# Optimization experiments

Hardware: AMD Instinct MI355X
Metric: run time of the kernel (lower is better)

## Reference

```python
import jax, jax.numpy as jnp
import numpy as np

B, L = 2, 4096
EMBED_DIM, NUM_HEADS, WINDOW = 1024, 16, 256
NUM_EXPERTS, TOP_K, FF_HIDDEN = 8, 2, 4096
ENTROPY_W, MAX_USAGE = 0.1, 0.3


def setup_inputs() -> dict:
    key = jax.random.key(0)
    ks = jax.random.split(key, 10)
    s = 0.02
    C, F, E = EMBED_DIM, FF_HIDDEN, NUM_EXPERTS
    return {
        "x": jax.random.normal(ks[0], (B, L, C), jnp.float32),
        "g1": jnp.ones((C,), jnp.float32), "b1": jnp.zeros((C,), jnp.float32),
        "g2": jnp.ones((C,), jnp.float32), "b2": jnp.zeros((C,), jnp.float32),
        "g3": jnp.ones((C,), jnp.float32), "b3": jnp.zeros((C,), jnp.float32),
        "Wqkv": jax.random.normal(ks[1], (C, 3 * C), jnp.float32) * s, "bqkv": jnp.zeros((3 * C,), jnp.float32),
        "Wo": jax.random.normal(ks[2], (C, C), jnp.float32) * s, "bo": jnp.zeros((C,), jnp.float32),
        "conv_w": jax.random.normal(ks[3], (C, C, 3), jnp.float32) * s, "conv_b": jnp.zeros((C,), jnp.float32),
        "gate_W": jax.random.normal(ks[4], (C, E), jnp.float32) * s, "gate_b": jnp.zeros((E,), jnp.float32),
        "expert_W": jax.random.normal(ks[5], (E, C, C), jnp.float32) * s, "expert_b": jnp.zeros((E, C), jnp.float32),
        "ff_W1": jax.random.normal(ks[6], (C, F), jnp.float32) * s, "ff_b1": jnp.zeros((F,), jnp.float32),
        "ff_W2": jax.random.normal(ks[7], (F, C), jnp.float32) * s, "ff_b2": jnp.zeros((C,), jnp.float32),
    }


def _ln(x, g, b):
    mu = x.mean(-1, keepdims=True)
    var = ((x - mu) ** 2).mean(-1, keepdims=True)
    return (x - mu) * jax.lax.rsqrt(var + 1e-5) * g + b


def _local_attn(x, Wqkv, bqkv, Wo, bo):
    # Faithful port of the unfold-based overlapping-window attention
    Bsz, Ln, C = x.shape
    hd = C // NUM_HEADS
    pad = (-Ln) % WINDOW
    xp = jnp.pad(x, ((0, 0), (0, pad), (0, 0)))
    Lp = Ln + pad
    qkv = (xp @ Wqkv + bqkv).reshape(Bsz, Lp, 3, NUM_HEADS, hd).transpose(2, 0, 3, 1, 4)
    q, k, v = qkv[0], qkv[1], qkv[2]  # [B,H,Lp,hd]
    step = WINDOW // 2  # bidirectional=True -> overlapping windows
    nw = (Lp - WINDOW) // step + 1
    idx = (jnp.arange(nw) * step)[:, None] + jnp.arange(WINDOW)[None, :]  # [nw,w]

    def win(t):
        # torch unfold(dim=2,size=w,step) puts window on LAST axis -> [B,H,nw,hd,w]
        return jnp.swapaxes(t[:, :, idx, :], -1, -2)

    qw, kw, vw = win(q), win(k), win(v)
    # q @ k^T over the window axis (exactly what the torch code computes)
    attn = jax.nn.softmax(jnp.einsum('bhnds,bhnes->bhnde', qw, kw) * hd ** -0.5, axis=-1)
    o = jnp.einsum('bhnde,bhnes->bhnds', attn, vw)  # [B,H,nw,hd,w]
    o = o.reshape(Bsz, NUM_HEADS, nw * WINDOW, hd).transpose(0, 2, 1, 3).reshape(Bsz, nw * WINDOW, C)
    return (o @ Wo + bo)[:, :Ln]


def _dconv(x, w, b):
    # Conv1d(C,C,k=3,dilation=2,padding='same'); w is [O,I,K]
    y = jax.lax.conv_general_dilated(jnp.swapaxes(x, 1, 2), w, (1,), 'SAME',
                                     rhs_dilation=(2,), dimension_numbers=('NCH', 'OIH', 'NCH'))
    return jnp.swapaxes(y + b[None, :, None], 1, 2)


def _moe(x, gW, gb, eW, eb):
    Bsz, S, C = x.shape
    N = Bsz * S
    xf = x.reshape(N, C)
    probs = jax.nn.softmax(xf @ gW + gb, axis=-1)
    entropy = -jnp.sum(probs * jnp.log(probs + 1e-10), axis=-1).mean()
    topk_p, topk_i = jax.lax.top_k(probs, TOP_K)  # [N,K]
    # dense-equivalent top-k dispatch: out[n] = sum_k p_k * expert_{i_k}(x_n)
    eo = jnp.einsum('nc,ech->neh', xf, eW) + eb  # [N,E,C]
    combine = jnp.zeros((N, NUM_EXPERTS), xf.dtype).at[jnp.arange(N)[:, None], topk_i].add(topk_p)
    out = jnp.einsum('neh,ne->nh', eo, combine)
    counts = jnp.zeros((NUM_EXPERTS,), jnp.float32).at[topk_i.reshape(-1)].add(1.0)
    penalty = jnp.sum(jax.nn.relu(counts / N - MAX_USAGE))
    return out.reshape(Bsz, S, C), ENTROPY_W * entropy + penalty


def reference(x, g1, b1, g2, b2, g3, b3, Wqkv, bqkv, Wo, bo, conv_w, conv_b,
              gate_W, gate_b, expert_W, expert_b, ff_W1, ff_b1, ff_W2, ff_b2):
    x = x + _local_attn(_ln(x, g1, b1), Wqkv, bqkv, Wo, bo)
    x = x + _dconv(_ln(x, g2, b2), conv_w, conv_b)
    moe_out, aux = _moe(_ln(x, g3, b3), gate_W, gate_b, expert_W, expert_b)
    x = x + moe_out
    x = x + (jax.nn.gelu(x @ ff_W1 + ff_b1, approximate=False) @ ff_W2 + ff_b2)
    return x, aux
```

## Files before the change

### kernel.cpp

```cpp
#include <hip/hip_runtime.h>
#include <cmath>

typedef _Float16 f16;
typedef __attribute__((ext_vector_type(8))) _Float16 f16x8;
typedef __attribute__((ext_vector_type(4))) _Float16 f16x4;
typedef __attribute__((ext_vector_type(4))) float f32x4;

struct TileInfo { int m0, mcnt, e, pad; };

__device__ __forceinline__ void gload16(const void* g, void* l) {
  __builtin_amdgcn_global_load_lds((const __attribute__((address_space(1))) void*)g,
                                   (__attribute__((address_space(3))) void*)l, 16, 0, 0);
}

__device__ __forceinline__ float fast_gelu(float u) {
  const float c = u * (0.7978845608028654f + 0.0356774081f * u * u);
  const float t = fminf(2.0f * c, 80.0f);
  const float e = __expf(t);
  return u * (e * __builtin_amdgcn_rcpf(e + 1.0f));
}

template<int NPASS, int MODE, int EPI>
__global__ __launch_bounds__(256)
void gemm_kernel(const f16* __restrict__ Ah, const f16* __restrict__ Al, int lda,
                 const f16* __restrict__ Bh, const f16* __restrict__ Bl, int ldb,
                 const float* __restrict__ bias, const float* __restrict__ res,
                 float* __restrict__ outf, f16* __restrict__ outh, int ldo, int K,
                 const int* __restrict__ rowmap, const TileInfo* __restrict__ table,
                 const char* __restrict__ zbuf) {
  __shared__ __align__(16) char lds[65536];

  const int tid  = threadIdx.x;
  const int wave = tid >> 6;
  const int lane = tid & 63;

  int m0, mcnt, eidx = 0;
  if (MODE == 2) {
    TileInfo ti = table[blockIdx.x];
    if (ti.mcnt <= 0) return;
    m0 = ti.m0; mcnt = ti.mcnt; eidx = ti.e;
  } else { m0 = blockIdx.x * 128; mcnt = 128; }
  const int n0 = blockIdx.y * 128;

  const f16* Bh_ = Bh;
  const float* bias_ = bias;
  size_t adelta = 0, bdelta = 0;
  if (NPASS == 3) {
    adelta = (size_t)((const char*)Al - (const char*)Ah);
    bdelta = (size_t)((const char*)Bl - (const char*)Bh);
  }
  if (MODE == 2) { Bh_ += ((size_t)eidx << 20); bias_ += eidx * 1024; }

  f32x4 acc[4][4] = {};
  const int wm  = (wave >> 1) * 64;
  const int wn  = (wave & 1) * 64;
  const int fr  = lane & 15;
  const int kgb = (lane >> 4) * 16;
  const int wuni = wave * 1024;

  const int sr    = tid / 8;
  const int cbyte = (tid % 8) * 16;

  if constexpr (NPASS == 1) {
    const char* aSrc[4];
    const char* bSrc[4];
    #pragma unroll
    for (int r = 0; r < 4; ++r) {
      const int mr  = sr + r * 32;
      const int cbs = cbyte ^ ((mr & 7) << 4);
      int gi = m0 + ((mr < mcnt) ? mr : (mcnt - 1));
      if (MODE == 1 || MODE == 2) gi = rowmap[gi];
      aSrc[r] = (const char*)Ah + (size_t)gi * lda * 2 + cbs;
      bSrc[r] = (const char*)Bh_ + (size_t)(n0 + mr) * ldb * 2 + cbs;
    }
    const int NT = K / 64;
    #pragma unroll
    for (int r = 0; r < 4; ++r) {
      gload16(aSrc[r], lds + r * 4096 + wuni);
      gload16(bSrc[r], lds + 16384 + r * 4096 + wuni);
    }
    #pragma unroll
    for (int r = 0; r < 4; ++r) {
      gload16(aSrc[r] + 128, lds + 32768 + r * 4096 + wuni);
      gload16(bSrc[r] + 128, lds + 32768 + 16384 + r * 4096 + wuni);
    }
    asm volatile("s_waitcnt vmcnt(8)" ::: "memory");
    __builtin_amdgcn_s_barrier();

    for (int kt = 0; kt < NT; ++kt) {
      const int c = kt & 1;
      const char* LAp = lds + c * 32768;
      const char* LBp = LAp + 16384;
      f16x8 ah[2][4], bh[2][4];
      #pragma unroll
      for (int kk = 0; kk < 2; ++kk) {
        #pragma unroll
        for (int i = 0; i < 4; ++i) {
          const int ar = wm + i * 16 + fr;
          ah[kk][i] = *(const f16x8*)(LAp + ar * 128 + ((kk * 64 + kgb) ^ ((ar & 7) << 4)));
          const int br = wn + i * 16 + fr;
          bh[kk][i] = *(const f16x8*)(LBp + br * 128 + ((kk * 64 + kgb) ^ ((br & 7) << 4)));
        }
      }
      asm volatile("s_waitcnt lgkmcnt(0)" ::: "memory");
      __builtin_amdgcn_s_barrier();
      if (kt + 2 < NT) {
        const size_t ko = (size_t)(kt + 2) * 128;
        #pragma unroll
        for (int r = 0; r < 4; ++r) {
          gload16(aSrc[r] + ko, lds + c * 32768 + r * 4096 + wuni);
          gload16(bSrc[r] + ko, lds + c * 32768 + 16384 + r * 4096 + wuni);
        }
      }
      #pragma unroll
      for (int kk = 0; kk < 2; ++kk)
        #pragma unroll
        for (int i = 0; i < 4; ++i)
          #pragma unroll
          for (int j = 0; j < 4; ++j)
            acc[i][j] = __builtin_amdgcn_mfma_f32_16x16x32_f16(ah[kk][i], bh[kk][j], acc[i][j], 0, 0, 0);
      if (kt + 2 < NT) asm volatile("s_waitcnt vmcnt(8)" ::: "memory");
      else             asm volatile("s_waitcnt vmcnt(0)" ::: "memory");
      __builtin_amdgcn_s_barrier();
    }
  } else {
    const char* aSrcB[4]; const char* bSrcB[4];
    int aRowC[4], aCbs[4];
    #pragma unroll
    for (int r = 0; r < 4; ++r) {
      const int mr  = sr + r * 32;
      const int cbs = cbyte ^ ((mr & 7) << 4);
      int gi = m0 + mr;
      if (MODE == 1) gi = rowmap[gi];
      if (MODE == 3) { aRowC[r] = gi; aCbs[r] = cbs; aSrcB[r] = nullptr; }
      else           { aSrcB[r] = (const char*)Ah + (size_t)gi * lda * 2 + cbs; aRowC[r] = 0; aCbs[r] = 0; }
      bSrcB[r] = (const char*)Bh_ + (size_t)(n0 + mr) * ldb * 2 + cbs;
    }
    for (int k0 = 0; k0 < K; k0 += 64) {
      #pragma unroll
      for (int r = 0; r < 4; ++r) {
        const char* as; const char* asl;
        if (MODE == 3) {
          const int tap = k0 >> 10;
          const int kc  = k0 & 1023;
          const int tok = aRowC[r] & 4095;
          const int stk = tok + (tap - 1) * 2;
          if (stk >= 0 && stk < 4096) {
            as  = (const char*)Ah + (size_t)(aRowC[r] + (tap - 1) * 2) * 2048 + kc * 2 + aCbs[r];
            asl = as + adelta;
          } else { as = zbuf; asl = zbuf; }
        } else {
          as  = aSrcB[r] + (size_t)k0 * 2;
          asl = as + adelta;
        }
        gload16(as,  lds + 0     + r * 4096 + wuni);
        gload16(asl, lds + 16384 + r * 4096 + wuni);
        const char* bs = bSrcB[r] + (size_t)k0 * 2;
        gload16(bs,          lds + 32768 + r * 4096 + wuni);
        gload16(bs + bdelta, lds + 49152 + r * 4096 + wuni);
      }
      __syncthreads();
      #pragma unroll
      for (int kk = 0; kk < 2; ++kk) {
        f16x8 ah[4], al[4], bh[4], bl[4];
        #pragma unroll
        for (int i = 0; i < 4; ++i) {
          const int ar = wm + i * 16 + fr;
          const int ao = ar * 128 + ((kk * 64 + kgb) ^ ((ar & 7) << 4));
          ah[i] = *(const f16x8*)(lds + ao);
          al[i] = *(const f16x8*)(lds + 16384 + ao);
          const int br = wn + i * 16 + fr;
          const int bo = br * 128 + ((kk * 64 + kgb) ^ ((br & 7) << 4));
          bh[i] = *(const f16x8*)(lds + 32768 + bo);
          bl[i] = *(const f16x8*)(lds + 49152 + bo);
        }
        #pragma unroll
        for (int i = 0; i < 4; ++i) {
          #pragma unroll
          for (int j = 0; j < 4; ++j) {
            acc[i][j] = __builtin_amdgcn_mfma_f32_16x16x32_f16(ah[i], bh[j], acc[i][j], 0, 0, 0);
            acc[i][j] = __builtin_amdgcn_mfma_f32_16x16x32_f16(ah[i], bl[j], acc[i][j], 0, 0, 0);
            acc[i][j] = __builtin_amdgcn_mfma_f32_16x16x32_f16(al[i], bh[j], acc[i][j], 0, 0, 0);
          }
        }
      }
      __syncthreads();
    }
  }

  #pragma unroll
  for (int i = 0; i < 4; ++i) {
    const int mb = wm + i * 16 + (lane >> 4) * 4;
    #pragma unroll
    for (int j = 0; j < 4; ++j) {
      const int nc = n0 + wn + j * 16 + fr;
      const float bv = bias_[nc];
      #pragma unroll
      for (int q = 0; q < 4; ++q) {
        const int ml = mb + q;
        if (MODE == 2 && ml >= mcnt) continue;
        const size_t orow = (size_t)(m0 + ml);
        float v = acc[i][j][q] + bv;
        if (EPI == 1) v += res[orow * ldo + nc];
        if (EPI == 3) v = fast_gelu(v);
        if (EPI <= 1) outf[orow * ldo + nc] = v;
        else          outh[orow * ldo + nc] = (f16)v;
      }
    }
  }
}

template<int WLO, int WGATE, int COMPACT>
__global__ __launch_bounds__(256)
void ln_kernel(const float* __restrict__ x, const float* __restrict__ g, const float* __restrict__ b,
               f16* __restrict__ oh, f16* __restrict__ ol,
               const float* __restrict__ gW, const float* __restrict__ gb,
               float* __restrict__ logits) {
  const int row = blockIdx.x;
  const int srow = COMPACT ? ((row < 2176) ? row : row + 1920) : row;
  const int t = threadIdx.x;
  const float4 v = ((const float4*)(x + (size_t)srow * 1024))[t];
  float s  = v.x + v.y + v.z + v.w;
  float ss = v.x * v.x + v.y * v.y + v.z * v.z + v.w * v.w;
  #pragma unroll
  for (int off = 32; off; off >>= 1) { s += __shfl_down(s, off, 64); ss += __shfl_down(ss, off, 64); }
  __shared__ float red[8];
  if ((t & 63) == 0) { red[t >> 6] = s; red[(t >> 6) + 4] = ss; }
  __syncthreads();
  s  = red[0] + red[1] + red[2] + red[3];
  ss = red[4] + red[5] + red[6] + red[7];
  const float mu  = s * (1.0f / 1024.0f);
  const float var = ss * (1.0f / 1024.0f) - mu * mu;
  const float inv = 1.0f / sqrtf(var + 1e-5f);
  const float4 gv = ((const float4*)g)[t];
  const float4 bv = ((const float4*)b)[t];
  float y[4];
  y[0] = (v.x - mu) * inv * gv.x + bv.x;
  y[1] = (v.y - mu) * inv * gv.y + bv.y;
  y[2] = (v.z - mu) * inv * gv.z + bv.z;
  y[3] = (v.w - mu) * inv * gv.w + bv.w;
  f16x4 hv;
  #pragma unroll
  for (int u = 0; u < 4; ++u) hv[u] = (f16)y[u];
  *(f16x4*)(oh + (size_t)row * 1024 + t * 4) = hv;
  if (WLO) {
    f16x4 lv;
    #pragma unroll
    for (int u = 0; u < 4; ++u) lv[u] = (f16)(y[u] - (float)hv[u]);
    *(f16x4*)(ol + (size_t)row * 1024 + t * 4) = lv;
  }
  if (WGATE) {
    const float* gr = gW + (size_t)(t * 4) * 8;
    float lg[8];
    #pragma unroll
    for (int e = 0; e < 8; ++e)
      lg[e] = y[0] * gr[e] + y[1] * gr[8 + e] + y[2] * gr[16 + e] + y[3] * gr[24 + e];
    #pragma unroll
    for (int m = 1; m < 64; m <<= 1)
      #pragma unroll
      for (int e = 0; e < 8; ++e) lg[e] += __shfl_xor(lg[e], m, 64);
    __shared__ float gred[4][8];
    if ((t & 63) == 0) {
      #pragma unroll
      for (int e = 0; e < 8; ++e) gred[t >> 6][e] = lg[e];
    }
    __syncthreads();
    if (t < 8)
      logits[(size_t)row * 8 + t] = gred[0][t] + gred[1][t] + gred[2][t] + gred[3][t] + gb[t];
  }
}

__global__ __launch_bounds__(512, 4)
void attn_kernel(const float* __restrict__ qkv, f16* __restrict__ oh, f16* __restrict__ ol) {
  __shared__ __align__(16) char sm[81920];
  const int bid = blockIdx.x;
  const int b = bid >> 8, h = (bid >> 4) & 15, n = bid & 15;
  const int t = threadIdx.x;
  const size_t rowbase = (size_t)(b * 2176 + n * 128);
  const char* qg = (const char*)(qkv + rowbase * 3072 + h * 64);
  const char* kg = qg + 4096;
  const char* vg = qg + 8192;

  const int srow = t >> 4;
  const int scol = (t & 15) * 16;
  const int wuni = (t >> 6) * 1024;

  const int dt = t >> 4;
  const int et = t & 15;
  float pacc[2][4] = {};

  for (int r = 0; r < 2; ++r) {
    #pragma unroll
    for (int p = 0; p < 4; ++p) {
      const size_t off = (size_t)(r * 128 + p * 32 + srow) * 12288 + scol;
      gload16(qg + off, sm + p * 8192 + wuni);
      gload16(kg + off, sm + 32768 + p * 8192 + wuni);
    }
    __syncthreads();
    #pragma unroll 4
    for (int s = 0; s < 128; ++s) {
      const float2 q2 = *(const float2*)(sm + s * 256 + dt * 8);
      const f32x4 k4 = *(const f32x4*)(sm + 32768 + s * 256 + et * 16);
      #pragma unroll
      for (int z = 0; z < 4; ++z) {
        pacc[0][z] += q2.x * k4[z];
        pacc[1][z] += q2.y * k4[z];
      }
    }
    __syncthreads();
  }

  #pragma unroll
  for (int i = 0; i < 2; ++i) {
    #pragma unroll
    for (int z = 0; z < 4; ++z) pacc[i][z] *= 0.125f;
    float m = fmaxf(fmaxf(pacc[i][0], pacc[i][1]), fmaxf(pacc[i][2], pacc[i][3]));
    m = fmaxf(m, __shfl_xor(m, 1, 16));
    m = fmaxf(m, __shfl_xor(m, 2, 16));
    m = fmaxf(m, __shfl_xor(m, 4, 16));
    m = fmaxf(m, __shfl_xor(m, 8, 16));
    float den = 0.0f;
    #pragma unroll
    for (int z = 0; z < 4; ++z) { pacc[i][z] = __expf(pacc[i][z] - m); den += pacc[i][z]; }
    den += __shfl_xor(den, 1, 16);
    den += __shfl_xor(den, 2, 16);
    den += __shfl_xor(den, 4, 16);
    den += __shfl_xor(den, 8, 16);
    const float dinv = 1.0f / den;
    f32x4 pv;
    #pragma unroll
    for (int z = 0; z < 4; ++z) pv[z] = pacc[i][z] * dinv;
    *(f32x4*)(sm + 65536 + (dt * 2 + i) * 256 + et * 16) = pv;
  }

  const int dt2 = t & 15;
  const int st  = t >> 4;
  const int ch  = h * 64 + (st & 15) * 4;
  const size_t rb2 = (size_t)(b * 4096 + n * 256);

  for (int c = 0; c < 2; ++c) {
    __syncthreads();
    #pragma unroll
    for (int p = 0; p < 4; ++p) {
      const size_t off = (size_t)(c * 128 + p * 32 + srow) * 12288 + scol;
      gload16(vg + off, sm + p * 8192 + wuni);
    }
    __syncthreads();
    float o[16];
    #pragma unroll
    for (int u = 0; u < 16; ++u) o[u] = 0.0f;
    #pragma unroll 2
    for (int e4 = 0; e4 < 16; ++e4) {
      f32x4 p4[4], v4[4];
      #pragma unroll
      for (int i = 0; i < 4; ++i)
        p4[i] = *(const f32x4*)(sm + 65536 + (dt2 * 4 + i) * 256 + e4 * 16);
      #pragma unroll
      for (int j = 0; j < 4; ++j)
        v4[j] = *(const f32x4*)(sm + (st * 4 + j) * 256 + e4 * 16);
      #pragma unroll
      for (int j = 0; j < 4; ++j)
        #pragma unroll
        for (int i = 0; i < 4; ++i) {
          o[j * 4 + i] += v4[j][0] * p4[i][0] + v4[j][1] * p4[i][1]
                        + v4[j][2] * p4[i][2] + v4[j][3] * p4[i][3];
        }
    }
    const int rq = c * 2 + (st >> 4);
    #pragma unroll
    for (int i = 0; i < 4; ++i) {
      const size_t row = rb2 + (size_t)(dt2 * 4 + i) * 4 + rq;
      f16x4 hv, lv;
      #pragma unroll
      for (int j = 0; j < 4; ++j) {
        const float val = o[j * 4 + i];
        hv[j] = (f16)val;
        lv[j] = (f16)(val - (float)hv[j]);
      }
      *(f16x4*)(oh + row * 1024 + ch) = hv;
      *(f16x4*)(ol + row * 1024 + ch) = lv;
    }
  }
}

template<int SPLIT>
__global__ __launch_bounds__(256)
void transpose_kernel(const float* __restrict__ in, int R, int Cc,
                      f16* __restrict__ oh, f16* __restrict__ ol) {
  __shared__ float tile[32][33];
  const size_t mat = (size_t)blockIdx.z * R * Cc;
  in += mat; oh += mat; if (SPLIT) ol += mat;
  const int tx = threadIdx.x & 31, ty = threadIdx.x >> 5;
  const int c = blockIdx.x * 32 + tx;
  #pragma unroll
  for (int j = 0; j < 32; j += 8) {
    const int r = blockIdx.y * 32 + ty + j;
    tile[ty + j][tx] = in[(size_t)r * Cc + c];
  }
  __syncthreads();
  const int rT = blockIdx.y * 32 + tx;
  #pragma unroll
  for (int j = 0; j < 32; j += 8) {
    const int cT = blockIdx.x * 32 + ty + j;
    const float v = tile[tx][ty + j];
    const f16 hv = (f16)v;
    oh[(size_t)cT * R + rT] = hv;
    if (SPLIT) ol[(size_t)cT * R + rT] = (f16)(v - (float)hv);
  }
}

__global__ __launch_bounds__(256)
void convw_kernel(const float* __restrict__ w, f16* __restrict__ oh, f16* __restrict__ ol) {
  const int id = blockIdx.x * 256 + threadIdx.x;
  const int o = id >> 10, i = id & 1023;
  const float* ws = w + (size_t)o * 3072 + i * 3;
  #pragma unroll
  for (int tap = 0; tap < 3; ++tap) {
    const float v = ws[tap];
    const f16 hv = (f16)v;
    const size_t oi = (size_t)o * 3072 + tap * 1024 + i;
    oh[oi] = hv;
    ol[oi] = (f16)(v - (float)hv);
  }
}

__global__ __launch_bounds__(256)
void gatefin_kernel(const float* __restrict__ logits, float* __restrict__ top2p,
                    int* __restrict__ top2i, float* __restrict__ ent,
                    int* __restrict__ counts) {
  __shared__ int hist[8];
  const int t = threadIdx.x;
  if (t < 8) hist[t] = 0;
  __syncthreads();
  const int token = blockIdx.x * 256 + t;
  float lg[8];
  const float4 l0 = ((const float4*)(logits + (size_t)token * 8))[0];
  const float4 l1 = ((const float4*)(logits + (size_t)token * 8))[1];
  lg[0] = l0.x; lg[1] = l0.y; lg[2] = l0.z; lg[3] = l0.w;
  lg[4] = l1.x; lg[5] = l1.y; lg[6] = l1.z; lg[7] = l1.w;
  int i0 = 0; float v0 = lg[0];
  #pragma unroll
  for (int e = 1; e < 8; ++e) if (lg[e] > v0) { v0 = lg[e]; i0 = e; }
  int i1 = 0; float v1 = -1e30f;
  #pragma unroll
  for (int e = 0; e < 8; ++e) if (e != i0 && lg[e] > v1) { v1 = lg[e]; i1 = e; }
  float den = 0.0f; float pr[8];
  #pragma unroll
  for (int e = 0; e < 8; ++e) { pr[e] = __expf(lg[e] - v0); den += pr[e]; }
  const float dinv = 1.0f / den;
  float H = 0.0f, p0 = 0.0f, p1 = 0.0f;
  #pragma unroll
  for (int e = 0; e < 8; ++e) {
    const float p = pr[e] * dinv;
    H -= p * __logf(p + 1e-10f);
    if (e == i0) p0 = p;
    if (e == i1) p1 = p;
  }
  ent[token] = H;
  top2p[token * 2] = p0; top2p[token * 2 + 1] = p1;
  top2i[token * 2] = i0; top2i[token * 2 + 1] = i1;
  atomicAdd(&hist[i0], 1);
  atomicAdd(&hist[i1], 1);
  __syncthreads();
  if (t < 8) atomicAdd(&counts[t], hist[t]);
}

__global__ __launch_bounds__(256)
void scan_kernel(const float* __restrict__ ent, const int* __restrict__ counts,
                 int* __restrict__ offs, TileInfo* __restrict__ table, float* __restrict__ auxout) {
  __shared__ float red[256];
  const int t = threadIdx.x;
  float s = 0.0f;
  for (int k = 0; k < 32; ++k) s += ent[t + (k << 8)];
  red[t] = s; __syncthreads();
  for (int hh = 128; hh > 0; hh >>= 1) { if (t < hh) red[t] += red[t + hh]; __syncthreads(); }
  if (t == 0) {
    const float entmean = red[0] * (1.0f / 8192.0f);
    float pen = 0.0f; int off = 0; int nt = 0;
    for (int e = 0; e < 8; ++e) {
      const int c = counts[e];
      offs[e] = off;
      for (int m = 0; m < c; m += 128) {
        table[nt].m0 = off + m;
        table[nt].mcnt = (c - m < 128) ? (c - m) : 128;
        table[nt].e = e; table[nt].pad = 0;
        ++nt;
      }
      off += c;
      const float fr = (float)c * (1.0f / 8192.0f) - 0.3f;
      pen += (fr > 0.0f) ? fr : 0.0f;
    }
    for (; nt < 160; ++nt) { table[nt].m0 = 0; table[nt].mcnt = 0; table[nt].e = 0; table[nt].pad = 0; }
    auxout[0] = 0.1f * entmean + pen;
  }
}

__global__ __launch_bounds__(256)
void scatter_kernel(const int* __restrict__ top2i, const int* __restrict__ offs,
                    int* __restrict__ fill, int* __restrict__ moe_rows,
                    int* __restrict__ row2slot) {
  __shared__ int hist[8];
  __shared__ int base[8];
  const int t = threadIdx.x;
  if (t < 8) hist[t] = 0;
  __syncthreads();
  const int id = blockIdx.x * 256 + t;
  const int e = top2i[id];
  const int myrank = atomicAdd(&hist[e], 1);
  __syncthreads();
  if (t < 8) base[t] = atomicAdd(&fill[t], hist[t]);
  __syncthreads();
  const int row = offs[e] + base[e] + myrank;
  moe_rows[row] = id >> 1;
  row2slot[id] = row;
}

__global__ __launch_bounds__(256)
void combine_kernel(const float* __restrict__ x2, const f16* __restrict__ eo,
                    const float* __restrict__ top2p, const int* __restrict__ row2slot,
                    float* __restrict__ x3, f16* __restrict__ x3h) {
  const int n = blockIdx.x;
  const int t = threadIdx.x;
  const int r0 = row2slot[n * 2], r1 = row2slot[n * 2 + 1];
  const float p0 = top2p[n * 2], p1 = top2p[n * 2 + 1];
  const float4 xv = ((const float4*)(x2 + (size_t)n * 1024))[t];
  const f16x4 e0 = ((const f16x4*)(eo + (size_t)r0 * 1024))[t];
  const f16x4 e1 = ((const f16x4*)(eo + (size_t)r1 * 1024))[t];
  float4 o;
  o.x = xv.x + p0 * (float)e0[0] + p1 * (float)e1[0];
  o.y = xv.y + p0 * (float)e0[1] + p1 * (float)e1[1];
  o.z = xv.z + p0 * (float)e0[2] + p1 * (float)e1[2];
  o.w = xv.w + p0 * (float)e0[3] + p1 * (float)e1[3];
  ((float4*)(x3 + (size_t)n * 1024))[t] = o;
  f16x4 hv; hv[0] = (f16)o.x; hv[1] = (f16)o.y; hv[2] = (f16)o.z; hv[3] = (f16)o.w;
  ((f16x4*)(x3h + (size_t)n * 1024))[t] = hv;
}

extern "C" void kernel_launch(void* const* d_in, const int* in_sizes, int n_in,
                              void* d_out, int out_size, void* d_ws, size_t ws_size,
                              hipStream_t stream) {
  (void)in_sizes; (void)n_in; (void)out_size; (void)ws_size;
  const float* x     = (const float*)d_in[0];
  const float* g1    = (const float*)d_in[1];
  const float* b1    = (const float*)d_in[2];
  const float* g2    = (const float*)d_in[3];
  const float* b2    = (const float*)d_in[4];
  const float* g3    = (const float*)d_in[5];
  const float* b3    = (const float*)d_in[6];
  const float* Wqkv  = (const float*)d_in[7];
  const float* bqkv  = (const float*)d_in[8];
  const float* Wo    = (const float*)d_in[9];
  const float* bo    = (const float*)d_in[10];
  const float* convw = (const float*)d_in[11];
  const float* convb = (const float*)d_in[12];
  const float* gateW = (const float*)d_in[13];
  const float* gateb = (const float*)d_in[14];
  const float* expW  = (const float*)d_in[15];
  const float* expb  = (const float*)d_in[16];
  const float* ffW1  = (const float*)d_in[17];
  const float* ffb1  = (const float*)d_in[18];
  const float* ffW2  = (const float*)d_in[19];
  const float* ffb2  = (const float*)d_in[20];
  float* out = (float*)d_out;

  char* W = (char*)d_ws;
  f16* wqkvT_h = (f16*)(W + 0);
  f16* wqkvT_l = (f16*)(W + 6291456);
  f16* woT_h   = (f16*)(W + 12582912);
  f16* woT_l   = (f16*)(W + 14680064);
  f16* wcvT_h  = (f16*)(W + 16777216);
  f16* wcvT_l  = (f16*)(W + 23068672);
  f16* wexpT   = (f16*)(W + 29360128);
  f16* wff1T   = (f16*)(W + 46137344);
  f16* wff2T   = (f16*)(W + 54525952);
  char* META   = W + 62914560;
  int* counts    = (int*)(META);
  int* fill      = (int*)(META + 32);
  int* offs      = (int*)(META + 64);
  TileInfo* table = (TileInfo*)(META + 128);
  char* zbuf     = META + 3072;
  float* ent     = (float*)(META + 24576);
  float* top2p   = (float*)(META + 57344);
  int* top2i     = (int*)(META + 122880);
  int* moe_rows  = (int*)(META + 188416);
  int* row2slot  = (int*)(META + 253952);
  float* logits  = (float*)(META + 327680);
  char* SA = W + 63963136;
  char* SB = W + 97517568;
  char* SC = W + 164626432;
  char* SD = W + 198180864;
  char* SE = W + 231735296;

  f16* ln1h = (f16*)SA;            f16* ln1l = (f16*)(SA + 16777216);
  f16* ln2h = ln1h;                f16* ln2l = ln1l;
  f16* ln3h = ln1h;                f16* x3h  = (f16*)(SA + 16777216);
  float* qkvbuf = (float*)SB;
  float* x2buf  = (float*)SB;
  f16*   hbuf   = (f16*)SB;
  f16* attnh = (f16*)SC;           f16* attnl = (f16*)(SC + 16777216);
  float* x1 = (float*)SD;
  f16* eobuf = (f16*)SD;
  float* x3 = (float*)SE;

  hipMemsetAsync((void*)META, 0, 4096, stream);

  dim3 blk(256);
  transpose_kernel<1><<<dim3(96, 32, 1), blk, 0, stream>>>(Wqkv, 1024, 3072, wqkvT_h, wqkvT_l);
  transpose_kernel<1><<<dim3(32, 32, 1), blk, 0, stream>>>(Wo, 1024, 1024, woT_h, woT_l);
  convw_kernel<<<4096, blk, 0, stream>>>(convw, wcvT_h, wcvT_l);
  transpose_kernel<0><<<dim3(32, 32, 8), blk, 0, stream>>>(expW, 1024, 1024, wexpT, nullptr);
  transpose_kernel<0><<<dim3(128, 32, 1), blk, 0, stream>>>(ffW1, 1024, 4096, wff1T, nullptr);
  transpose_kernel<0><<<dim3(32, 128, 1), blk, 0, stream>>>(ffW2, 4096, 1024, wff2T, nullptr);

  ln_kernel<1, 0, 1><<<4352, blk, 0, stream>>>(x, g1, b1, ln1h, ln1l, nullptr, nullptr, nullptr);
  gemm_kernel<3, 0, 0><<<dim3(34, 24), blk, 0, stream>>>(ln1h, ln1l, 1024, wqkvT_h, wqkvT_l, 1024,
      bqkv, nullptr, qkvbuf, nullptr, 3072, 1024, nullptr, nullptr, nullptr);
  attn_kernel<<<512, dim3(512), 0, stream>>>(qkvbuf, attnh, attnl);
  gemm_kernel<3, 0, 1><<<dim3(64, 8), blk, 0, stream>>>(attnh, attnl, 1024, woT_h, woT_l, 1024,
      bo, x, x1, nullptr, 1024, 1024, nullptr, nullptr, nullptr);
  ln_kernel<1, 0, 0><<<8192, blk, 0, stream>>>(x1, g2, b2, ln2h, ln2l, nullptr, nullptr, nullptr);
  gemm_kernel<3, 3, 1><<<dim3(64, 8), blk, 0, stream>>>(ln2h, ln2l, 1024, wcvT_h, wcvT_l, 3072,
      convb, x1, x2buf, nullptr, 1024, 3072, nullptr, nullptr, zbuf);
  ln_kernel<0, 1, 0><<<8192, blk, 0, stream>>>(x2buf, g3, b3, ln3h, nullptr, gateW, gateb, logits);
  gatefin_kernel<<<32, blk, 0, stream>>>(logits, top2p, top2i, ent, counts);
  scan_kernel<<<1, blk, 0, stream>>>(ent, counts, offs, table, out + 8388608);
  scatter_kernel<<<64, blk, 0, stream>>>(top2i, offs, fill, moe_rows, row2slot);
  gemm_kernel<1, 2, 2><<<dim3(136, 8), blk, 0, stream>>>(ln3h, nullptr, 1024, wexpT, nullptr, 1024,
      expb, nullptr, nullptr, eobuf, 1024, 1024, moe_rows, table, nullptr);
  combine_kernel<<<8192, blk, 0, stream>>>(x2buf, eobuf, top2p, row2slot, x3, x3h);
  gemm_kernel<1, 0, 3><<<dim3(64, 32), blk, 0, stream>>>(x3h, nullptr, 1024, wff1T, nullptr, 1024,
      ffb1, nullptr, nullptr, hbuf, 4096, 1024, nullptr, nullptr, nullptr);
  gemm_kernel<1, 0, 1><<<dim3(64, 8), blk, 0, stream>>>(hbuf, nullptr, 4096, wff2T, nullptr, 4096,
      ffb2, x3, out, nullptr, 1024, 4096, nullptr, nullptr, nullptr);
}
```

Measured before the change: 743.9 us.

## Fuse weight prep, LN1 and meta zeroing into one kernel; drop fp32 x3

Merges the six weight transpose/convert launches, the first layernorm and the metadata memset into a single prep kernel that dispatches on block index. It also merges the scan and scatter kernels into one launch. Separately, the combine step no longer writes an fp32 x3; the final FF2 GEMM reads the fp16 x3h as its residual through a new epilogue mode. This cuts launch overhead and an 32MB fp32 write/read, at the cost of residual precision (fp16 residual added to the output).

```diff
diff --git a/kernel.cpp b/kernel.cpp
--- a/kernel.cpp
+++ b/kernel.cpp
@@ -202,29 +202,29 @@
         const size_t orow = (size_t)(m0 + ml);
         float v = acc[i][j][q] + bv;
         if (EPI == 1) v += res[orow * ldo + nc];
+        if (EPI == 4) v += (float)((const f16*)res)[orow * ldo + nc];
         if (EPI == 3) v = fast_gelu(v);
-        if (EPI <= 1) outf[orow * ldo + nc] = v;
-        else          outh[orow * ldo + nc] = (f16)v;
-      }
-    }
-  }
-}
-
-template<int WLO, int WGATE, int COMPACT>
-__global__ __launch_bounds__(256)
-void ln_kernel(const float* __restrict__ x, const float* __restrict__ g, const float* __restrict__ b,
-               f16* __restrict__ oh, f16* __restrict__ ol,
-               const float* __restrict__ gW, const float* __restrict__ gb,
-               float* __restrict__ logits) {
-  const int row = blockIdx.x;
-  const int srow = COMPACT ? ((row < 2176) ? row : row + 1920) : row;
+        if (EPI <= 1 || EPI == 4) outf[orow * ldo + nc] = v;
+        else                      outh[orow * ldo + nc] = (f16)v;
+      }
+    }
+  }
+}
+
+template<int WLO, int WGATE>
+__device__ __forceinline__ void ln_body(const float* __restrict__ x, int srow, int row,
+    const float* __restrict__ g, const float* __restrict__ b,
+    f16* __restrict__ oh, f16* __restrict__ ol,
+    const float* __restrict__ gW, const float* __restrict__ gb,
+    float* __restrict__ logits, char* smraw) {
+  float* red  = (float*)smraw;
+  float* gred = (float*)(smraw + 32);
   const int t = threadIdx.x;
   const float4 v = ((const float4*)(x + (size_t)srow * 1024))[t];
   float s  = v.x + v.y + v.z + v.w;
   float ss = v.x * v.x + v.y * v.y + v.z * v.z + v.w * v.w;
   #pragma unroll
   for (int off = 32; off; off >>= 1) { s += __shfl_down(s, off, 64); ss += __shfl_down(ss, off, 64); }
-  __shared__ float red[8];
   if ((t & 63) == 0) { red[t >> 6] = s; red[(t >> 6) + 4] = ss; }
   __syncthreads();
   s  = red[0] + red[1] + red[2] + red[3];
@@ -259,15 +259,94 @@
     for (int m = 1; m < 64; m <<= 1)
       #pragma unroll
       for (int e = 0; e < 8; ++e) lg[e] += __shfl_xor(lg[e], m, 64);
-    __shared__ float gred[4][8];
     if ((t & 63) == 0) {
       #pragma unroll
-      for (int e = 0; e < 8; ++e) gred[t >> 6][e] = lg[e];
+      for (int e = 0; e < 8; ++e) gred[(t >> 6) * 8 + e] = lg[e];
     }
     __syncthreads();
     if (t < 8)
-      logits[(size_t)row * 8 + t] = gred[0][t] + gred[1][t] + gred[2][t] + gred[3][t] + gb[t];
-  }
+      logits[(size_t)row * 8 + t] = gred[t] + gred[8 + t] + gred[16 + t] + gred[24 + t] + gb[t];
+  }
+}
+
+template<int WLO, int WGATE>
+__global__ __launch_bounds__(256)
+void ln_kernel(const float* __restrict__ x, const float* __restrict__ g, const float* __restrict__ b,
+               f16* __restrict__ oh, f16* __restrict__ ol,
+               const float* __restrict__ gW, const float* __restrict__ gb,
+               float* __restrict__ logits) {
+  __shared__ __align__(16) char sm[160];
+  ln_body<WLO, WGATE>(x, blockIdx.x, blockIdx.x, g, b, oh, ol, gW, gb, logits, sm);
+}
+
+template<int SPLIT>
+__device__ __forceinline__ void transpose_body(const float* __restrict__ in, int R, int Cc,
+    f16* __restrict__ oh, f16* __restrict__ ol, int bx, int by, int z, char* smraw) {
+  float (*tile)[33] = (float(*)[33])smraw;
+  const size_t mat = (size_t)z * R * Cc;
+  in += mat; oh += mat; if (SPLIT) ol += mat;
+  const int tx = threadIdx.x & 31, ty = threadIdx.x >> 5;
+  const int c = bx * 32 + tx;
+  #pragma unroll
+  for (int j = 0; j < 32; j += 8) {
+    const int r = by * 32 + ty + j;
+    tile[ty + j][tx] = in[(size_t)r * Cc + c];
+  }
+  __syncthreads();
+  const int rT = by * 32 + tx;
+  #pragma unroll
+  for (int j = 0; j < 32; j += 8) {
+    const int cT = bx * 32 + ty + j;
+    const float v = tile[tx][ty + j];
+    const f16 hv = (f16)v;
+    oh[(size_t)cT * R + rT] = hv;
+    if (SPLIT) ol[(size_t)cT * R + rT] = (f16)(v - (float)hv);
+  }
+}
+
+__global__ __launch_bounds__(256)
+void prep_kernel(const float* __restrict__ Wqkv, const float* __restrict__ Wo,
+                 const float* __restrict__ convw, const float* __restrict__ expW,
+                 const float* __restrict__ ffW1, const float* __restrict__ ffW2,
+                 f16* wqkvT_h, f16* wqkvT_l, f16* woT_h, f16* woT_l,
+                 f16* wcvT_h, f16* wcvT_l, f16* wexpT, f16* wff1T, f16* wff2T,
+                 const float* __restrict__ x, const float* __restrict__ g1,
+                 const float* __restrict__ b1, f16* ln1h, f16* ln1l,
+                 char* __restrict__ meta) {
+  __shared__ __align__(16) char sm[4224];
+  int bid = blockIdx.x;
+  if (bid < 3072) { transpose_body<1>(Wqkv, 1024, 3072, wqkvT_h, wqkvT_l, bid % 96, bid / 96, 0, sm); return; }
+  bid -= 3072;
+  if (bid < 1024) { transpose_body<1>(Wo, 1024, 1024, woT_h, woT_l, bid & 31, bid >> 5, 0, sm); return; }
+  bid -= 1024;
+  if (bid < 4096) {
+    const int id = bid * 256 + threadIdx.x;
+    const int o = id >> 10, i = id & 1023;
+    const float* ws = convw + (size_t)o * 3072 + i * 3;
+    #pragma unroll
+    for (int tap = 0; tap < 3; ++tap) {
+      const float v = ws[tap];
+      const f16 hv = (f16)v;
+      const size_t oi = (size_t)o * 3072 + tap * 1024 + i;
+      wcvT_h[oi] = hv;
+      wcvT_l[oi] = (f16)(v - (float)hv);
+    }
+    return;
+  }
+  bid -= 4096;
+  if (bid < 8192) { const int z = bid >> 10, r = bid & 1023; transpose_body<0>(expW, 1024, 1024, wexpT, nullptr, r & 31, r >> 5, z, sm); return; }
+  bid -= 8192;
+  if (bid < 4096) { transpose_body<0>(ffW1, 1024, 4096, wff1T, nullptr, bid & 127, bid >> 7, 0, sm); return; }
+  bid -= 4096;
+  if (bid < 4096) { transpose_body<0>(ffW2, 4096, 1024, wff2T, nullptr, bid & 31, bid >> 5, 0, sm); return; }
+  bid -= 4096;
+  if (bid < 4352) {
+    const int srow = (bid < 2176) ? bid : bid + 1920;
+    ln_body<1, 0>(x, srow, bid, g1, b1, ln1h, ln1l, nullptr, nullptr, nullptr, sm);
+    return;
+  }
+  f32x4 z4 = {0.0f, 0.0f, 0.0f, 0.0f};
+  ((f32x4*)meta)[threadIdx.x] = z4;
 }
 
 __global__ __launch_bounds__(512, 4)
@@ -380,47 +459,6 @@
       *(f16x4*)(oh + row * 1024 + ch) = hv;
       *(f16x4*)(ol + row * 1024 + ch) = lv;
     }
-  }
-}
-
-template<int SPLIT>
-__global__ __launch_bounds__(256)
-void transpose_kernel(const float* __restrict__ in, int R, int Cc,
-                      f16* __restrict__ oh, f16* __restrict__ ol) {
-  __shared__ float tile[32][33];
-  const size_t mat = (size_t)blockIdx.z * R * Cc;
-  in += mat; oh += mat; if (SPLIT) ol += mat;
-  const int tx = threadIdx.x & 31, ty = threadIdx.x >> 5;
-  const int c = blockIdx.x * 32 + tx;
-  #pragma unroll
-  for (int j = 0; j < 32; j += 8) {
-    const int r = blockIdx.y * 32 + ty + j;
-    tile[ty + j][tx] = in[(size_t)r * Cc + c];
-  }
-  __syncthreads();
-  const int rT = blockIdx.y * 32 + tx;
-  #pragma unroll
-  for (int j = 0; j < 32; j += 8) {
-    const int cT = blockIdx.x * 32 + ty + j;
-    const float v = tile[tx][ty + j];
-    const f16 hv = (f16)v;
-    oh[(size_t)cT * R + rT] = hv;
-    if (SPLIT) ol[(size_t)cT * R + rT] = (f16)(v - (float)hv);
-  }
-}
-
-__global__ __launch_bounds__(256)
-void convw_kernel(const float* __restrict__ w, f16* __restrict__ oh, f16* __restrict__ ol) {
-  const int id = blockIdx.x * 256 + threadIdx.x;
-  const int o = id >> 10, i = id & 1023;
-  const float* ws = w + (size_t)o * 3072 + i * 3;
-  #pragma unroll
-  for (int tap = 0; tap < 3; ++tap) {
-    const float v = ws[tap];
-    const f16 hv = (f16)v;
-    const size_t oi = (size_t)o * 3072 + tap * 1024 + i;
-    oh[oi] = hv;
-    ol[oi] = (f16)(v - (float)hv);
   }
 }
 
@@ -466,42 +504,16 @@
 }
 
 __global__ __launch_bounds__(256)
-void scan_kernel(const float* __restrict__ ent, const int* __restrict__ counts,
-                 int* __restrict__ offs, TileInfo* __restrict__ table, float* __restrict__ auxout) {
+void scatter_fused(const float* __restrict__ ent, const int* __restrict__ counts,
+                   const int* __restrict__ top2i, int* __restrict__ fill,
+                   int* __restrict__ moe_rows, int* __restrict__ row2slot,
+                   TileInfo* __restrict__ table, float* __restrict__ auxout) {
+  __shared__ int loffs[8];
+  __shared__ int hist[8];
+  __shared__ int base[8];
   __shared__ float red[256];
   const int t = threadIdx.x;
-  float s = 0.0f;
-  for (int k = 0; k < 32; ++k) s += ent[t + (k << 8)];
-  red[t] = s; __syncthreads();
-  for (int hh = 128; hh > 0; hh >>= 1) { if (t < hh) red[t] += red[t + hh]; __syncthreads(); }
-  if (t == 0) {
-    const float entmean = red[0] * (1.0f / 8192.0f);
-    float pen = 0.0f; int off = 0; int nt = 0;
-    for (int e = 0; e < 8; ++e) {
-      const int c = counts[e];
-      offs[e] = off;
-      for (int m = 0; m < c; m += 128) {
-        table[nt].m0 = off + m;
-        table[nt].mcnt = (c - m < 128) ? (c - m) : 128;
-        table[nt].e = e; table[nt].pad = 0;
-        ++nt;
-      }
-      off += c;
-      const float fr = (float)c * (1.0f / 8192.0f) - 0.3f;
-      pen += (fr > 0.0f) ? fr : 0.0f;
-    }
-    for (; nt < 160; ++nt) { table[nt].m0 = 0; table[nt].mcnt = 0; table[nt].e = 0; table[nt].pad = 0; }
-    auxout[0] = 0.1f * entmean + pen;
-  }
-}
-
-__global__ __launch_bounds__(256)
-void scatter_kernel(const int* __restrict__ top2i, const int* __restrict__ offs,
-                    int* __restrict__ fill, int* __restrict__ moe_rows,
-                    int* __restrict__ row2slot) {
-  __shared__ int hist[8];
-  __shared__ int base[8];
-  const int t = threadIdx.x;
+  if (t == 0) { int off = 0; for (int e = 0; e < 8; ++e) { loffs[e] = off; off += counts[e]; } }
   if (t < 8) hist[t] = 0;
   __syncthreads();
   const int id = blockIdx.x * 256 + t;
@@ -510,15 +522,38 @@
   __syncthreads();
   if (t < 8) base[t] = atomicAdd(&fill[t], hist[t]);
   __syncthreads();
-  const int row = offs[e] + base[e] + myrank;
+  const int row = loffs[e] + base[e] + myrank;
   moe_rows[row] = id >> 1;
   row2slot[id] = row;
+  if (blockIdx.x == 0) {
+    float s = 0.0f;
+    for (int k = 0; k < 32; ++k) s += ent[t + (k << 8)];
+    red[t] = s; __syncthreads();
+    for (int hh = 128; hh > 0; hh >>= 1) { if (t < hh) red[t] += red[t + hh]; __syncthreads(); }
+    if (t == 0) {
+      const float entmean = red[0] * (1.0f / 8192.0f);
+      float pen = 0.0f; int nt = 0;
+      for (int e2 = 0; e2 < 8; ++e2) {
+        const int c = counts[e2];
+        for (int m = 0; m < c; m += 128) {
+          table[nt].m0 = loffs[e2] + m;
+          table[nt].mcnt = (c - m < 128) ? (c - m) : 128;
+          table[nt].e = e2; table[nt].pad = 0;
+          ++nt;
+        }
+        const float fr = (float)c * (1.0f / 8192.0f) - 0.3f;
+        pen += (fr > 0.0f) ? fr : 0.0f;
+      }
+      for (; nt < 160; ++nt) { table[nt].m0 = 0; table[nt].mcnt = 0; table[nt].e = 0; table[nt].pad = 0; }
+      auxout[0] = 0.1f * entmean + pen;
+    }
+  }
 }
 
 __global__ __launch_bounds__(256)
 void combine_kernel(const float* __restrict__ x2, const f16* __restrict__ eo,
                     const float* __restrict__ top2p, const int* __restrict__ row2slot,
-                    float* __restrict__ x3, f16* __restrict__ x3h) {
+                    f16* __restrict__ x3h) {
   const int n = blockIdx.x;
   const int t = threadIdx.x;
   const int r0 = row2slot[n * 2], r1 = row2slot[n * 2 + 1];
@@ -526,13 +561,11 @@
   const float4 xv = ((const float4*)(x2 + (size_t)n * 1024))[t];
   const f16x4 e0 = ((const f16x4*)(eo + (size_t)r0 * 1024))[t];
   const f16x4 e1 = ((const f16x4*)(eo + (size_t)r1 * 1024))[t];
-  float4 o;
-  o.x = xv.x + p0 * (float)e0[0] + p1 * (float)e1[0];
-  o.y = xv.y + p0 * (float)e0[1] + p1 * (float)e1[1];
-  o.z = xv.z + p0 * (float)e0[2] + p1 * (float)e1[2];
-  o.w = xv.w + p0 * (float)e0[3] + p1 * (float)e1[3];
-  ((float4*)(x3 + (size_t)n * 1024))[t] = o;
-  f16x4 hv; hv[0] = (f16)o.x; hv[1] = (f16)o.y; hv[2] = (f16)o.z; hv[3] = (f16)o.w;
+  f16x4 hv;
+  hv[0] = (f16)(xv.x + p0 * (float)e0[0] + p1 * (float)e1[0]);
+  hv[1] = (f16)(xv.y + p0 * (float)e0[1] + p1 * (float)e1[1]);
+  hv[2] = (f16)(xv.z + p0 * (float)e0[2] + p1 * (float)e1[2]);
+  hv[3] = (f16)(xv.w + p0 * (float)e0[3] + p1 * (float)e1[3]);
   ((f16x4*)(x3h + (size_t)n * 1024))[t] = hv;
 }
 
@@ -576,7 +609,6 @@
   char* META   = W + 62914560;
   int* counts    = (int*)(META);
   int* fill      = (int*)(META + 32);
-  int* offs      = (int*)(META + 64);
   TileInfo* table = (TileInfo*)(META + 128);
   char* zbuf     = META + 3072;
   float* ent     = (float*)(META + 24576);
@@ -589,7 +621,6 @@
   char* SB = W + 97517568;
   char* SC = W + 164626432;
   char* SD = W + 198180864;
-  char* SE = W + 231735296;
 
   f16* ln1h = (f16*)SA;            f16* ln1l = (f16*)(SA + 16777216);
   f16* ln2h = ln1h;                f16* ln2l = ln1l;
@@ -600,36 +631,28 @@
   f16* attnh = (f16*)SC;           f16* attnl = (f16*)(SC + 16777216);
   float* x1 = (float*)SD;
   f16* eobuf = (f16*)SD;
-  float* x3 = (float*)SE;
-
-  hipMemsetAsync((void*)META, 0, 4096, stream);
 
   dim3 blk(256);
-  transpose_kernel<1><<<dim3(96, 32, 1), blk, 0, stream>>>(Wqkv, 1024, 3072, wqkvT_h, wqkvT_l);
-  transpose_kernel<1><<<dim3(32, 32, 1), blk, 0, stream>>>(Wo, 1024, 1024, woT_h, woT_l);
-  convw_kernel<<<4096, blk, 0, stream>>>(convw, wcvT_h, wcvT_l);
-  transpose_kernel<0><<<dim3(32, 32, 8), blk, 0, stream>>>(expW, 1024, 1024, wexpT, nullptr);
-  transpose_kernel<0><<<dim3(128, 32, 1), blk, 0, stream>>>(ffW1, 1024, 4096, wff1T, nullptr);
-  transpose_kernel<0><<<dim3(32, 128, 1), blk, 0, stream>>>(ffW2, 4096, 1024, wff2T, nullptr);
-
-  ln_kernel<1, 0, 1><<<4352, blk, 0, stream>>>(x, g1, b1, ln1h, ln1l, nullptr, nullptr, nullptr);
+  prep_kernel<<<28929, blk, 0, stream>>>(Wqkv, Wo, convw, expW, ffW1, ffW2,
+      wqkvT_h, wqkvT_l, woT_h, woT_l, wcvT_h, wcvT_l, wexpT, wff1T, wff2T,
+      x, g1, b1, ln1h, ln1l, META);
   gemm_kernel<3, 0, 0><<<dim3(34, 24), blk, 0, stream>>>(ln1h, ln1l, 1024, wqkvT_h, wqkvT_l, 1024,
       bqkv, nullptr, qkvbuf, nullptr, 3072, 1024, nullptr, nullptr, nullptr);
   attn_kernel<<<512, dim3(512), 0, stream>>>(qkvbuf, attnh, attnl);
   gemm_kernel<3, 0, 1><<<dim3(64, 8), blk, 0, stream>>>(attnh, attnl, 1024, woT_h, woT_l, 1024,
       bo, x, x1, nullptr, 1024, 1024, nullptr, nullptr, nullptr);
-  ln_kernel<1, 0, 0><<<8192, blk, 0, stream>>>(x1, g2, b2, ln2h, ln2l, nullptr, nullptr, nullptr);
+  ln_kernel<1, 0><<<8192, blk, 0, stream>>>(x1, g2, b2, ln2h, ln2l, nullptr, nullptr, nullptr);
   gemm_kernel<3, 3, 1><<<dim3(64, 8), blk, 0, stream>>>(ln2h, ln2l, 1024, wcvT_h, wcvT_l, 3072,
       convb, x1, x2buf, nullptr, 1024, 3072, nullptr, nullptr, zbuf);
-  ln_kernel<0, 1, 0><<<8192, blk, 0, stream>>>(x2buf, g3, b3, ln3h, nullptr, gateW, gateb, logits);
+  ln_kernel<0, 1><<<8192, blk, 0, stream>>>(x2buf, g3, b3, ln3h, nullptr, gateW, gateb, logits);
   gatefin_kernel<<<32, blk, 0, stream>>>(logits, top2p, top2i, ent, counts);
-  scan_kernel<<<1, blk, 0, stream>>>(ent, counts, offs, table, out + 8388608);
-  scatter_kernel<<<64, blk, 0, stream>>>(top2i, offs, fill, moe_rows, row2slot);
+  scatter_fused<<<64, blk, 0, stream>>>(ent, counts, top2i, fill, moe_rows, row2slot,
+      table, out + 8388608);
   gemm_kernel<1, 2, 2><<<dim3(136, 8), blk, 0, stream>>>(ln3h, nullptr, 1024, wexpT, nullptr, 1024,
       expb, nullptr, nullptr, eobuf, 1024, 1024, moe_rows, table, nullptr);
-  combine_kernel<<<8192, blk, 0, stream>>>(x2buf, eobuf, top2p, row2slot, x3, x3h);
+  combine_kernel<<<8192, blk, 0, stream>>>(x2buf, eobuf, top2p, row2slot, x3h);
   gemm_kernel<1, 0, 3><<<dim3(64, 32), blk, 0, stream>>>(x3h, nullptr, 1024, wff1T, nullptr, 1024,
       ffb1, nullptr, nullptr, hbuf, 4096, 1024, nullptr, nullptr, nullptr);
-  gemm_kernel<1, 0, 1><<<dim3(64, 8), blk, 0, stream>>>(hbuf, nullptr, 4096, wff2T, nullptr, 4096,
-      ffb2, x3, out, nullptr, 1024, 4096, nullptr, nullptr, nullptr);
-}
+  gemm_kernel<1, 0, 4><<<dim3(64, 8), blk, 0, stream>>>(hbuf, nullptr, 4096, wff2T, nullptr, 4096,
+      ffb2, (const float*)x3h, out, nullptr, 1024, 4096, nullptr, nullptr, nullptr);
+}
```

After: 669.6 us, median of 2. -10.0%, faster.
